# Optimization experiments

Hardware: AMD Instinct MI355X
Metric: run time of the kernel (lower is better)

## Reference

```python
import jax, jax.numpy as jnp
import numpy as np

K_HOPS = 2  # number_layers


def _gcn_norm(edge_index, edge_weight, num_nodes):
    # add self loops with weight 1 (PyG gcn_norm default, fill_value=1)
    row, col = edge_index[0], edge_index[1]
    loop = jnp.arange(num_nodes, dtype=edge_index.dtype)
    row = jnp.concatenate([row, loop])
    col = jnp.concatenate([col, loop])
    w = jnp.concatenate([edge_weight, jnp.ones((num_nodes,), edge_weight.dtype)])
    deg = jax.ops.segment_sum(w, col, num_segments=num_nodes)
    dinv = jnp.where(deg > 0, jax.lax.rsqrt(deg), 0.0)
    norm = dinv[row] * w * dinv[col]
    return row, col, norm


def setup_inputs() -> dict:
    key = jax.random.key(0)
    k1, k2, k3, k4 = jax.random.split(key, 4)
    N, E, F_IN, F_OUT = 100000, 1600000, 256, 40
    x = jax.random.normal(k1, (N, F_IN), dtype=jnp.float32)
    edge_index = jax.random.randint(k2, (2, E), 0, N, dtype=jnp.int64)
    edge_attr = jax.random.uniform(k3, (E,), dtype=jnp.float32)
    W = jax.random.normal(k4, (F_OUT, F_IN), dtype=jnp.float32) * (1.0 / np.sqrt(F_IN))
    b = jnp.zeros((F_OUT,), dtype=jnp.float32)
    return {"x": x, "edge_index": edge_index, "edge_attr": edge_attr, "W": W, "b": b}


def reference(x, edge_index, edge_attr, W, b):
    N = x.shape[0]
    row, col, norm = _gcn_norm(edge_index, edge_attr, N)
    for _ in range(K_HOPS):
        x = jax.ops.segment_sum(norm[:, None] * x[row], col, num_segments=N)
    out = x @ W.T + b           # SGConv final linear
    out = jax.nn.relu(out)      # dropout is a no-op in eval mode
    return jax.nn.log_softmax(out, axis=-1)
```

## Files before the change

kernel.cpp:

```cpp
#include <hip/hip_runtime.h>
#include <hip/hip_bf16.h>
#include <math.h>

#define TF_IN   256
#define TF_OUT  40
#define NCH2    5
#define BCAP    48
#define WQ      32767.0f
#define BIN_SHIFT 8
#define MAXBINS 512
#define EPB 4096


struct us8 { ushort4 a, b; };

__device__ inline float bf2f(unsigned short u) {
    union { unsigned int i; float f; } t; t.i = ((unsigned int)u) << 16; return t.f;
}
__device__ inline unsigned short f2bf(float f) {
    union { float f; unsigned int i; } t; t.f = f;
    unsigned int r = t.i + 0x7FFF + ((t.i >> 16) & 1);
    return (unsigned short)(r >> 16);
}

__device__ inline void acc8(float* acc, float v, const us8& h) {
    acc[0] += v * bf2f(h.a.x); acc[1] += v * bf2f(h.a.y);
    acc[2] += v * bf2f(h.a.z); acc[3] += v * bf2f(h.a.w);
    acc[4] += v * bf2f(h.b.x); acc[5] += v * bf2f(h.b.y);
    acc[6] += v * bf2f(h.b.z); acc[7] += v * bf2f(h.b.w);
}

__global__ void zero_kernel(int* __restrict__ a, int na, int* __restrict__ b, int nb) {
    int i = blockIdx.x * blockDim.x + threadIdx.x;
    if (i < na) a[i] = 0;
    if (i < nb) b[i] = 0;
}

__global__ __launch_bounds__(256) void partition_kernel(
        const int* __restrict__ row, const int* __restrict__ col,
        const float* __restrict__ w, int* __restrict__ binCnt,
        uint2* __restrict__ bins, int E, int bincap, int nbins) {
    __shared__ int hist[MAXBINS];
    __shared__ unsigned int cursor[MAXBINS];
    int tid = threadIdx.x;
    int base = (int)blockIdx.x * EPB;

    for (int i = tid; i < nbins; i += 256) hist[i] = 0;

    int   ec[16], er[16];
    float ev[16];
#pragma unroll
    for (int i = 0; i < 16; ++i) ec[i] = -1;
#pragma unroll
    for (int q = 0; q < 4; ++q) {
        int e = base + (q * 256 + tid) * 4;
        if (e + 4 <= E) {
            int4   c4 = *(const int4*)(col + e);
            int4   r4 = *(const int4*)(row + e);
            float4 w4 = *(const float4*)(w + e);
            ec[q * 4 + 0] = c4.x; ec[q * 4 + 1] = c4.y; ec[q * 4 + 2] = c4.z; ec[q * 4 + 3] = c4.w;
            er[q * 4 + 0] = r4.x; er[q * 4 + 1] = r4.y; er[q * 4 + 2] = r4.z; er[q * 4 + 3] = r4.w;
            ev[q * 4 + 0] = w4.x; ev[q * 4 + 1] = w4.y; ev[q * 4 + 2] = w4.z; ev[q * 4 + 3] = w4.w;
        } else {
            for (int j = 0; j < 4; ++j) {
                int ee = e + j;
                if (ee < E) { ec[q * 4 + j] = col[ee]; er[q * 4 + j] = row[ee]; ev[q * 4 + j] = w[ee]; }
            }
        }
    }
    __syncthreads();

#pragma unroll
    for (int i = 0; i < 16; ++i)
        if (ec[i] >= 0) atomicAdd(&hist[ec[i] >> BIN_SHIFT], 1);
    __syncthreads();

    for (int bq = tid; bq < nbins; bq += 256) {
        int hc = hist[bq];
        unsigned int g = (unsigned int)bq * (unsigned int)bincap;
        if (hc > 0) g += (unsigned int)atomicAdd(&binCnt[bq], hc);
        cursor[bq] = g;
    }
    __syncthreads();

#pragma unroll
    for (int i = 0; i < 16; ++i) {
        if (ec[i] >= 0) {
            int bq = ec[i] >> BIN_SHIFT;
            unsigned int p = atomicAdd(&cursor[bq], 1u);
            if (p < (unsigned int)(bq + 1) * (unsigned int)bincap) {
                unsigned int wq = (unsigned int)(ev[i] * WQ + 0.5f);
                uint2 ent; ent.x = ((unsigned int)er[i] << 15) | wq; ent.y = (unsigned int)ec[i];
                bins[p] = ent;
            }
        }
    }
}

__global__ __launch_bounds__(256) void fused_gemm_binscatter_kernel(
        const float* __restrict__ x, const float* __restrict__ W,
        unsigned short* __restrict__ h, int N, int nbins,
        const int* __restrict__ binCnt, const uint2* __restrict__ bins, int bincap,
        int* __restrict__ cnt, unsigned int* __restrict__ bucket) {
    __shared__ float4 xs[128][8];
    __shared__ float4 wsm[40][9];
    int tid = threadIdx.x;

    if ((int)blockIdx.x < nbins) {
        int b = blockIdx.x;
        int mb = binCnt[b]; if (mb > bincap) mb = bincap;
        const uint2* src = bins + (size_t)b * bincap;
        for (int i = tid; i < mb; i += 256) {
            uint2 e = src[i];
            int c = (int)e.y;
            int pos = atomicAdd(&cnt[c], 1);
            if (pos < BCAP) bucket[(size_t)c * BCAP + pos] = e.x;
        }
    } else {
        int q = (int)blockIdx.x - nbins;
        int ng = tid >> 2;
        int jg = tid & 3;
        int j0 = jg * 10;
        int nodeBase = q * 128;
        int sk = (ng >> 1) & 7;

        float acc[2][10];
#pragma unroll
        for (int i = 0; i < 2; ++i)
#pragma unroll
            for (int j = 0; j < 10; ++j) acc[i][j] = 0.f;

        const float4* x4 = (const float4*)x;
        const float4* W4 = (const float4*)W;

        for (int kt = 0; kt < 8; ++kt) {
            int kb4 = kt * 8;
#pragma unroll
            for (int i = 0; i < 4; ++i) {
                int idx = tid + i * 256;
                int n = idx >> 3, c4 = idx & 7;
                int gn = nodeBase + n;
                float4 v = make_float4(0.f, 0.f, 0.f, 0.f);
                if (gn < N) v = x4[(size_t)gn * (TF_IN / 4) + kb4 + c4];
                xs[n][c4 ^ ((n >> 2) & 7)] = v;
            }
            {
                int idx = tid;
                int j = idx >> 3, c4 = idx & 7;
                wsm[j][c4] = W4[(size_t)j * (TF_IN / 4) + kb4 + c4];
                if (tid < 64) {
                    idx = tid + 256;
                    j = idx >> 3; c4 = idx & 7;
                    wsm[j][c4] = W4[(size_t)j * (TF_IN / 4) + kb4 + c4];
                }
            }
            __syncthreads();
#pragma unroll 2
            for (int c4 = 0; c4 < 8; ++c4) {
                int phys = c4 ^ sk;
                float4 xv0 = xs[ng * 2][phys];
                float4 xv1 = xs[ng * 2 + 1][phys];
#pragma unroll
                for (int jj = 0; jj < 10; ++jj) {
                    float4 wv = wsm[j0 + jj][c4];
                    acc[0][jj] += xv0.x * wv.x + xv0.y * wv.y + xv0.z * wv.z + xv0.w * wv.w;
                    acc[1][jj] += xv1.x * wv.x + xv1.y * wv.y + xv1.z * wv.z + xv1.w * wv.w;
                }
            }
            __syncthreads();
        }

#pragma unroll
        for (int i = 0; i < 2; ++i) {
            int gn = nodeBase + ng * 2 + i;
            if (gn < N) {
                ushort2* hp2 = (ushort2*)(h + (size_t)gn * TF_OUT + j0);
#pragma unroll
                for (int p = 0; p < 5; ++p) {
                    ushort2 o;
                    o.x = f2bf(acc[i][2 * p]);
                    o.y = f2bf(acc[i][2 * p + 1]);
                    hp2[p] = o;
                }
            }
        }
    }
}

__global__ void deg_kernel(const unsigned int* __restrict__ bucket, const int* __restrict__ cnt,
                           float* __restrict__ dinv, int N) {
    int n = blockIdx.x * blockDim.x + threadIdx.x;
    if (n >= N) return;
    int m = cnt[n]; if (m > BCAP) m = BCAP;
    const unsigned int* b = bucket + (size_t)n * BCAP;
    unsigned int si = 0;
    int k = 0;
    for (; k + 4 <= m; k += 4) {
        uint4 e4 = *(const uint4*)(b + k);
        si += (e4.x & 0x7FFF) + (e4.y & 0x7FFF) + (e4.z & 0x7FFF) + (e4.w & 0x7FFF);
    }
    for (; k < m; ++k) si += b[k] & 0x7FFF;
    float s = 1.0f + (float)si * (1.0f / WQ);
    dinv[n] = rsqrtf(s);
}

__device__ inline void stage_rv(int g, int chunk, int m,
                                const unsigned int* __restrict__ b,
                                const float* __restrict__ dinv,
                                int rs[64][BCAP + 1], float vs[64][BCAP + 1]) {
    int k0 = chunk * 10;
    unsigned int e[10];
#pragma unroll
    for (int i = 0; i < 10; ++i) {
        int k = k0 + i;
        e[i] = (k < m) ? b[k] : 0u;
    }
    float dv[10];
#pragma unroll
    for (int i = 0; i < 10; ++i) dv[i] = dinv[e[i] >> 15];
#pragma unroll
    for (int i = 0; i < 10; ++i) {
        int k = k0 + i;
        if (k < m) {
            rs[g][k] = (int)(e[i] >> 15);
            vs[g][k] = dv[i] * ((float)(e[i] & 0x7FFF) * (1.0f / WQ));
        }
    }
}

__device__ inline void gather_lds(float* acc, const us8* __restrict__ hin,
                                  int g, int chunk, int m,
                                  const int rs[64][BCAP + 1], const float vs[64][BCAP + 1]) {
    int k = 0;
    for (; k + 4 <= m; k += 4) {
        int r0 = rs[g][k],     r1 = rs[g][k + 1];
        int r2 = rs[g][k + 2], r3 = rs[g][k + 3];
        us8 h0 = hin[(size_t)r0 * NCH2 + chunk];
        us8 h1 = hin[(size_t)r1 * NCH2 + chunk];
        us8 h2 = hin[(size_t)r2 * NCH2 + chunk];
        us8 h3 = hin[(size_t)r3 * NCH2 + chunk];
        acc8(acc, vs[g][k],     h0); acc8(acc, vs[g][k + 1], h1);
        acc8(acc, vs[g][k + 2], h2); acc8(acc, vs[g][k + 3], h3);
    }
    for (; k < m; ++k) {
        us8 hv = hin[(size_t)rs[g][k] * NCH2 + chunk];
        acc8(acc, vs[g][k], hv);
    }
}

__global__ __launch_bounds__(320) void hop_bf_kernel(
        const us8* __restrict__ hin, us8* __restrict__ hout,
        const int* __restrict__ cnt, const unsigned int* __restrict__ bucket,
        const float* __restrict__ dinv, int N) {
    __shared__ int   rs[64][BCAP + 1];
    __shared__ float vs[64][BCAP + 1];
    int tid = threadIdx.x;
    int g = tid / NCH2;
    int chunk = tid - g * NCH2;
    int node = blockIdx.x * 64 + g;

    int m = 0;
    float d = 0.f;
    if (node < N) {
        m = cnt[node]; if (m > BCAP) m = BCAP;
        d = dinv[node];
        stage_rv(g, chunk, m, bucket + (size_t)node * BCAP, dinv, rs, vs);
    }
    __syncthreads();
    if (node >= N) return;

    us8 a = hin[(size_t)node * NCH2 + chunk];
    float acc[8];
    acc[0] = bf2f(a.a.x) * d; acc[1] = bf2f(a.a.y) * d;
    acc[2] = bf2f(a.a.z) * d; acc[3] = bf2f(a.a.w) * d;
    acc[4] = bf2f(a.b.x) * d; acc[5] = bf2f(a.b.y) * d;
    acc[6] = bf2f(a.b.z) * d; acc[7] = bf2f(a.b.w) * d;

    gather_lds(acc, hin, g, chunk, m, rs, vs);

    us8 o;
    o.a.x = f2bf(acc[0] * d); o.a.y = f2bf(acc[1] * d);
    o.a.z = f2bf(acc[2] * d); o.a.w = f2bf(acc[3] * d);
    o.b.x = f2bf(acc[4] * d); o.b.y = f2bf(acc[5] * d);
    o.b.z = f2bf(acc[6] * d); o.b.w = f2bf(acc[7] * d);
    hout[(size_t)node * NCH2 + chunk] = o;
}

__global__ __launch_bounds__(320) void hop2_epi_kernel(
        const us8* __restrict__ hin, float4* __restrict__ out,
        const int* __restrict__ cnt, const unsigned int* __restrict__ bucket,
        const float* __restrict__ dinv, const float* __restrict__ bias, int N) {
    __shared__ int   rs[64][BCAP + 1];
    __shared__ float vs[64][BCAP + 1];
    __shared__ float redm[320];
    __shared__ float reds[320];
    int tid = threadIdx.x;
    int g = tid / NCH2;
    int chunk = tid - g * NCH2;
    int node = blockIdx.x * 64 + g;
    bool valid = node < N;

    int m = 0;
    float d = 0.f;
    if (valid) {
        m = cnt[node]; if (m > BCAP) m = BCAP;
        d = dinv[node];
        stage_rv(g, chunk, m, bucket + (size_t)node * BCAP, dinv, rs, vs);
    }
    __syncthreads();

    float acc[8];
#pragma unroll
    for (int j = 0; j < 8; ++j) acc[j] = 0.f;
    if (valid) {
        us8 a = hin[(size_t)node * NCH2 + chunk];
        acc[0] = bf2f(a.a.x) * d; acc[1] = bf2f(a.a.y) * d;
        acc[2] = bf2f(a.a.z) * d; acc[3] = bf2f(a.a.w) * d;
        acc[4] = bf2f(a.b.x) * d; acc[5] = bf2f(a.b.y) * d;
        acc[6] = bf2f(a.b.z) * d; acc[7] = bf2f(a.b.w) * d;
        gather_lds(acc, hin, g, chunk, m, rs, vs);
    }

    float v[8];
    float lm = -1e30f;
    if (valid) {
#pragma unroll
        for (int j = 0; j < 8; ++j) {
            float t2 = acc[j] * d + bias[chunk * 8 + j];
            t2 = fmaxf(t2, 0.f);
            v[j] = t2;
            lm = fmaxf(lm, t2);
        }
    }
    redm[tid] = lm;
    __syncthreads();
    float gm = redm[g * NCH2];
#pragma unroll
    for (int i = 1; i < NCH2; ++i) gm = fmaxf(gm, redm[g * NCH2 + i]);

    float ps = 0.f;
    if (valid) {
#pragma unroll
        for (int j = 0; j < 8; ++j) ps += __expf(v[j] - gm);
    }
    reds[tid] = ps;
    __syncthreads();
    float s = reds[g * NCH2];
#pragma unroll
    for (int i = 1; i < NCH2; ++i) s += reds[g * NCH2 + i];
    float lse = gm + __logf(s);

    if (valid) {
        float4 o0 = make_float4(v[0] - lse, v[1] - lse, v[2] - lse, v[3] - lse);
        float4 o1 = make_float4(v[4] - lse, v[5] - lse, v[6] - lse, v[7] - lse);
        out[(size_t)node * 10 + chunk * 2]     = o0;
        out[(size_t)node * 10 + chunk * 2 + 1] = o1;
    }
}

extern "C" void kernel_launch(void* const* d_in, const int* in_sizes, int n_in,
                              void* d_out, int out_size, void* d_ws, size_t ws_size,
                              hipStream_t stream) {
    const float* x  = (const float*)d_in[0];
    const int*   ei = (const int*)d_in[1];
    const float* ew = (const float*)d_in[2];
    const float* W  = (const float*)d_in[3];
    const float* b  = (const float*)d_in[4];

    const int F_out = in_sizes[4];
    const int F_in  = in_sizes[3] / F_out;
    const int N     = in_sizes[0] / F_in;
    const int E     = in_sizes[2];
    const int* row = ei;
    const int* col = ei + E;

    char* ws = (char*)d_ws;
    size_t off = 0;
    auto alloc = [&](size_t bytes) {
        void* p = ws + off;
        off += (bytes + 255) & ~(size_t)255;
        return p;
    };

    int*          cnt    = (int*)          alloc((size_t)N * 4);
    float*        dinv   = (float*)        alloc((size_t)N * 4);
    unsigned int* bucket = (unsigned int*) alloc((size_t)N * BCAP * 4);
    unsigned short* h0   = (unsigned short*)alloc((size_t)N * TF_OUT * 2);
    unsigned short* h1   = (unsigned short*)alloc((size_t)N * TF_OUT * 2);
    int nbins = (N + (1 << BIN_SHIFT) - 1) >> BIN_SHIFT;
    int* binCnt = (int*)alloc((size_t)nbins * 4);

    size_t outBytes = (size_t)N * F_out * 4;
    int bincap = (int)(outBytes / ((size_t)nbins * 8));
    uint2* bins = (uint2*)d_out;

    const int tb = 256;
    hipLaunchKernelGGL(zero_kernel, dim3((N + tb - 1) / tb), dim3(tb), 0, stream,
                       cnt, N, binCnt, nbins);

    int partBlocks = (E + EPB - 1) / EPB;
    hipLaunchKernelGGL(partition_kernel, dim3(partBlocks), dim3(tb), 0, stream,
                       row, col, ew, binCnt, bins, E, bincap, nbins);

    int gemmBlocks = (N + 127) / 128;
    hipLaunchKernelGGL(fused_gemm_binscatter_kernel, dim3(nbins + gemmBlocks), dim3(256),
                       0, stream, x, W, h0, N, nbins, binCnt, bins, bincap, cnt, bucket);

    hipLaunchKernelGGL(deg_kernel, dim3((N + tb - 1) / tb), dim3(tb), 0, stream,
                       bucket, cnt, dinv, N);

    int hopBlocks = (N + 63) / 64;
    hipLaunchKernelGGL(hop_bf_kernel, dim3(hopBlocks), dim3(320), 0, stream,
                       (const us8*)h0, (us8*)h1, cnt, bucket, dinv, N);

    hipLaunchKernelGGL(hop2_epi_kernel, dim3(hopBlocks), dim3(320), 0, stream,
                       (const us8*)h1, (float4*)d_out, cnt, bucket, dinv, b, N);
}
```

Before: 332.4 us.

## Restructure GEMM to per-thread node rows with split-K across waves

Rewrites the x·Wᵀ GEMM so each thread owns one node and reads its x row directly from global memory, while the four waves split the K dimension and each wave reads W from LDS as broadcasts. Partial sums are reduced through LDS float atomics before the bf16 store, and blocks now cover 64 nodes instead of 128. This removes the x staging through LDS and most of the barriers. In exchange it needs 40 accumulators per thread, costs LDS atomic reductions, and has each lane make strided per-row global loads rather than coalesced ones.

```diff
diff --git a/kernel.cpp b/kernel.cpp
--- a/kernel.cpp
+++ b/kernel.cpp
@@ -97,13 +97,13 @@
     }
 }
 
-__global__ __launch_bounds__(256) void fused_gemm_binscatter_kernel(
+__global__ __launch_bounds__(256, 4) void fused_gemm_binscatter_kernel(
         const float* __restrict__ x, const float* __restrict__ W,
         unsigned short* __restrict__ h, int N, int nbins,
         const int* __restrict__ binCnt, const uint2* __restrict__ bins, int bincap,
         int* __restrict__ cnt, unsigned int* __restrict__ bucket) {
-    __shared__ float4 xs[128][8];
-    __shared__ float4 wsm[40][9];
+    __shared__ float4 wlds[1280];
+    __shared__ float  accs[64][41];
     int tid = threadIdx.x;
 
     if ((int)blockIdx.x < nbins) {
@@ -117,71 +117,67 @@
             if (pos < BCAP) bucket[(size_t)c * BCAP + pos] = e.x;
         }
     } else {
-        int q = (int)blockIdx.x - nbins;
-        int ng = tid >> 2;
-        int jg = tid & 3;
-        int j0 = jg * 10;
-        int nodeBase = q * 128;
-        int sk = (ng >> 1) & 7;
-
-        float acc[2][10];
-#pragma unroll
-        for (int i = 0; i < 2; ++i)
-#pragma unroll
-            for (int j = 0; j < 10; ++j) acc[i][j] = 0.f;
+        int blk = (int)blockIdx.x - nbins;
+        int nodeBase = blk * 64;
+        int wv = tid >> 6;
+        int ln = tid & 63;
+        int gn = nodeBase + ln;
+        bool valid = gn < N;
+
+        float acc[40];
+#pragma unroll
+        for (int j = 0; j < 40; ++j) acc[j] = 0.f;
+
+        for (int i = tid; i < 64 * 41; i += 256) ((float*)accs)[i] = 0.f;
 
         const float4* x4 = (const float4*)x;
         const float4* W4 = (const float4*)W;
-
-        for (int kt = 0; kt < 8; ++kt) {
-            int kb4 = kt * 8;
-#pragma unroll
-            for (int i = 0; i < 4; ++i) {
-                int idx = tid + i * 256;
-                int n = idx >> 3, c4 = idx & 7;
-                int gn = nodeBase + n;
-                float4 v = make_float4(0.f, 0.f, 0.f, 0.f);
-                if (gn < N) v = x4[(size_t)gn * (TF_IN / 4) + kb4 + c4];
-                xs[n][c4 ^ ((n >> 2) & 7)] = v;
-            }
-            {
-                int idx = tid;
-                int j = idx >> 3, c4 = idx & 7;
-                wsm[j][c4] = W4[(size_t)j * (TF_IN / 4) + kb4 + c4];
-                if (tid < 64) {
-                    idx = tid + 256;
-                    j = idx >> 3; c4 = idx & 7;
-                    wsm[j][c4] = W4[(size_t)j * (TF_IN / 4) + kb4 + c4];
+        int wb = wv * 8;
+
+        for (int half = 0; half < 2; ++half) {
+            __syncthreads();
+            for (int i = tid; i < 1280; i += 256)
+                wlds[i] = W4[(i >> 5) * 64 + half * 32 + (i & 31)];
+            __syncthreads();
+
+            const float4* xr = x4 + ((size_t)gn << 6) + half * 32 + wb;
+#pragma unroll
+            for (int kb = 0; kb < 2; ++kb) {
+                float4 xv0, xv1, xv2, xv3;
+                if (valid) {
+                    xv0 = xr[kb * 4 + 0]; xv1 = xr[kb * 4 + 1];
+                    xv2 = xr[kb * 4 + 2]; xv3 = xr[kb * 4 + 3];
+                } else {
+                    xv0 = xv1 = xv2 = xv3 = make_float4(0.f, 0.f, 0.f, 0.f);
+                }
+#pragma unroll
+                for (int j = 0; j < 40; ++j) {
+                    float4 w0 = wlds[j * 32 + wb + kb * 4 + 0];
+                    float4 w1 = wlds[j * 32 + wb + kb * 4 + 1];
+                    float4 w2 = wlds[j * 32 + wb + kb * 4 + 2];
+                    float4 w3 = wlds[j * 32 + wb + kb * 4 + 3];
+                    acc[j] += xv0.x * w0.x + xv0.y * w0.y + xv0.z * w0.z + xv0.w * w0.w
+                            + xv1.x * w1.x + xv1.y * w1.y + xv1.z * w1.z + xv1.w * w1.w
+                            + xv2.x * w2.x + xv2.y * w2.y + xv2.z * w2.z + xv2.w * w2.w
+                            + xv3.x * w3.x + xv3.y * w3.y + xv3.z * w3.z + xv3.w * w3.w;
                 }
             }
-            __syncthreads();
-#pragma unroll 2
-            for (int c4 = 0; c4 < 8; ++c4) {
-                int phys = c4 ^ sk;
-                float4 xv0 = xs[ng * 2][phys];
-                float4 xv1 = xs[ng * 2 + 1][phys];
-#pragma unroll
-                for (int jj = 0; jj < 10; ++jj) {
-                    float4 wv = wsm[j0 + jj][c4];
-                    acc[0][jj] += xv0.x * wv.x + xv0.y * wv.y + xv0.z * wv.z + xv0.w * wv.w;
-                    acc[1][jj] += xv1.x * wv.x + xv1.y * wv.y + xv1.z * wv.z + xv1.w * wv.w;
-                }
-            }
-            __syncthreads();
-        }
-
-#pragma unroll
-        for (int i = 0; i < 2; ++i) {
-            int gn = nodeBase + ng * 2 + i;
-            if (gn < N) {
-                ushort2* hp2 = (ushort2*)(h + (size_t)gn * TF_OUT + j0);
-#pragma unroll
-                for (int p = 0; p < 5; ++p) {
-                    ushort2 o;
-                    o.x = f2bf(acc[i][2 * p]);
-                    o.y = f2bf(acc[i][2 * p + 1]);
-                    hp2[p] = o;
-                }
+        }
+
+#pragma unroll
+        for (int j = 0; j < 40; ++j) atomicAdd(&accs[ln][j], acc[j]);
+        __syncthreads();
+
+        int n2 = tid >> 2, jg = tid & 3, j0 = jg * 10;
+        int g2 = nodeBase + n2;
+        if (g2 < N) {
+            ushort2* hp2 = (ushort2*)(h + (size_t)g2 * TF_OUT + j0);
+#pragma unroll
+            for (int p = 0; p < 5; ++p) {
+                ushort2 o;
+                o.x = f2bf(accs[n2][j0 + 2 * p]);
+                o.y = f2bf(accs[n2][j0 + 2 * p + 1]);
+                hp2[p] = o;
             }
         }
     }
@@ -402,7 +398,7 @@
     hipLaunchKernelGGL(partition_kernel, dim3(partBlocks), dim3(tb), 0, stream,
                        row, col, ew, binCnt, bins, E, bincap, nbins);
 
-    int gemmBlocks = (N + 127) / 128;
+    int gemmBlocks = (N + 63) / 64;
     hipLaunchKernelGGL(fused_gemm_binscatter_kernel, dim3(nbins + gemmBlocks), dim3(256),
                        0, stream, x, W, h0, N, nbins, binCnt, bins, bincap, cnt, bucket);
 
```

After: 1.255 ms. +277.4%, slower.
